# Kernel tuning notes

Hardware: AMD Instinct MI355X
Metric: run time of the kernel (lower is better)

Reference implementation:

```python
import jax, jax.numpy as jnp
import numpy as np

N = 50000   # nodes
E = 300000  # directed edges (~Delaunay mesh, degree 6)
H = 128     # hidden_size
TW = 5      # time_window
P = 3       # process_steps
NODE_IN = 9
EDGE_IN = 4
LN_EPS = 1e-5


def _ln(x, g, b):
    m = jnp.mean(x, axis=-1, keepdims=True)
    v = jnp.var(x, axis=-1, keepdims=True)
    return (x - m) * jax.lax.rsqrt(v + LN_EPS) * g + b


def _mlp_ln(x, w1, b1, w2, b2, g, bb):
    # Linear -> ReLU -> Linear -> LayerNorm (matches MLP(..., layer_norm=True))
    h = jax.nn.relu(x @ w1 + b1)
    return _ln(h @ w2 + b2, g, bb)


def setup_inputs() -> dict:
    key = jax.random.key(0)
    ks = iter(jax.random.split(key, 64))
    def nrm(shape):
        return jax.random.normal(next(ks), shape, jnp.float32)
    def lin(fi, fo, stack=None):
        sh = (fi, fo) if stack is None else (stack, fi, fo)
        return nrm(sh) / np.sqrt(fi)
    inp = {}
    inp["temperature"] = nrm((N,))
    inp["temperature_prev"] = nrm((N,))
    inp["heat_source"] = nrm((N,))
    inp["heat_source_prev"] = nrm((N,))
    inp["heat_source_next"] = nrm((N, TW))
    inp["mesh_pos"] = jax.random.uniform(next(ks), (N, 2), jnp.float32)
    inp["edge_index"] = jax.random.randint(next(ks), (2, E), 0, N, jnp.int32)
    # Normalizer params (running mean/std)
    inp["node_norm_mean"] = jnp.zeros((NODE_IN,), jnp.float32)
    inp["node_norm_std"] = jnp.ones((NODE_IN,), jnp.float32)
    inp["edge_norm_mean"] = jnp.zeros((EDGE_IN,), jnp.float32)
    inp["edge_norm_std"] = jnp.ones((EDGE_IN,), jnp.float32)
    # node encoder
    inp["ne_w1"] = lin(NODE_IN, H); inp["ne_b1"] = jnp.zeros((H,), jnp.float32)
    inp["ne_w2"] = lin(H, H);       inp["ne_b2"] = jnp.zeros((H,), jnp.float32)
    inp["ne_g"] = jnp.ones((H,), jnp.float32); inp["ne_be"] = jnp.zeros((H,), jnp.float32)
    # edge encoder
    inp["ee_w1"] = lin(EDGE_IN, H); inp["ee_b1"] = jnp.zeros((H,), jnp.float32)
    inp["ee_w2"] = lin(H, H);       inp["ee_b2"] = jnp.zeros((H,), jnp.float32)
    inp["ee_g"] = jnp.ones((H,), jnp.float32); inp["ee_be"] = jnp.zeros((H,), jnp.float32)
    # processors (stacked over P steps): edge_mlp in=3H, node_mlp in=2H
    inp["pe_w1"] = lin(3 * H, H, P); inp["pe_b1"] = jnp.zeros((P, H), jnp.float32)
    inp["pe_w2"] = lin(H, H, P);     inp["pe_b2"] = jnp.zeros((P, H), jnp.float32)
    inp["pe_g"] = jnp.ones((P, H), jnp.float32); inp["pe_be"] = jnp.zeros((P, H), jnp.float32)
    inp["pn_w1"] = lin(2 * H, H, P); inp["pn_b1"] = jnp.zeros((P, H), jnp.float32)
    inp["pn_w2"] = lin(H, H, P);     inp["pn_b2"] = jnp.zeros((P, H), jnp.float32)
    inp["pn_g"] = jnp.ones((P, H), jnp.float32); inp["pn_be"] = jnp.zeros((P, H), jnp.float32)
    # decoder (Conv1d kernel_size=1 == per-node Linear), Swish in between
    inp["dec_w1"] = lin(H, H // 2); inp["dec_b1"] = jnp.zeros((H // 2,), jnp.float32)
    inp["dec_w2"] = lin(H // 2, TW); inp["dec_b2"] = jnp.zeros((TW,), jnp.float32)
    return inp


def reference(temperature, temperature_prev, heat_source, heat_source_prev,
              heat_source_next, mesh_pos, edge_index,
              node_norm_mean, node_norm_std, edge_norm_mean, edge_norm_std,
              ne_w1, ne_b1, ne_w2, ne_b2, ne_g, ne_be,
              ee_w1, ee_b1, ee_w2, ee_b2, ee_g, ee_be,
              pe_w1, pe_b1, pe_w2, pe_b2, pe_g, pe_be,
              pn_w1, pn_b1, pn_w2, pn_b2, pn_g, pn_be,
              dec_w1, dec_b1, dec_w2, dec_b2):
    u = temperature
    # node features: [u, u_dot, q, q_dot, q_next]  -> [N, 9]
    x = jnp.concatenate([
        u[:, None], (u - temperature_prev)[:, None],
        heat_source[:, None], (heat_source - heat_source_prev)[:, None],
        heat_source_next], axis=-1)
    s, r = edge_index[0], edge_index[1]  # senders (source j), receivers (target i)
    rel = mesh_pos[s] - mesh_pos[r]                       # [E, 2]
    dist = jnp.linalg.norm(rel, axis=-1, keepdims=True)   # [E, 1]
    relt = (u[s] - u[r])[:, None]                         # [E, 1]
    e = jnp.concatenate([rel, dist, relt], axis=-1)       # [E, 4]

    xh = _mlp_ln((x - node_norm_mean) / node_norm_std, ne_w1, ne_b1, ne_w2, ne_b2, ne_g, ne_be)
    eh = _mlp_ln((e - edge_norm_mean) / edge_norm_std, ee_w1, ee_b1, ee_w2, ee_b2, ee_g, ee_be)

    n_nodes = xh.shape[0]
    for i in range(P):
        xs, xr = xh[s], xh[r]  # x_j = x[source], x_i = x[target]
        # message: edge_mlp(cat[x_i, x_j, e]) then scatter-add at target index
        msg = _mlp_ln(jnp.concatenate([xr, xs, eh], axis=-1),
                      pe_w1[i], pe_b1[i], pe_w2[i], pe_b2[i], pe_g[i], pe_be[i])
        aggr = jax.ops.segment_sum(msg, r, num_segments=n_nodes)
        # node update + residual
        new_x = _mlp_ln(jnp.concatenate([aggr, xh], axis=-1),
                        pn_w1[i], pn_b1[i], pn_w2[i], pn_b2[i], pn_g[i], pn_be[i]) + xh
        # edge update (note row/col ordering differs from message) + residual
        new_e = _mlp_ln(jnp.concatenate([xs, xr, eh], axis=-1),
                        pe_w1[i], pe_b1[i], pe_w2[i], pe_b2[i], pe_g[i], pe_be[i]) + eh
        xh, eh = new_x, new_e

    # decoder: 1x1 convs == per-node linears, Swish(beta=1) activation
    h = xh @ dec_w1 + dec_b1
    h = h * jax.nn.sigmoid(h)
    delta = (h @ dec_w2 + dec_b2).reshape(-1, TW)
    dt = jnp.arange(1, TW + 1, dtype=delta.dtype)
    return dt[None, :] * delta
```

## Files before the change

kernel.cpp:

```cpp
#include <hip/hip_runtime.h>
#include <stdint.h>

typedef unsigned short u16;
typedef __attribute__((ext_vector_type(8))) short bf16x8_t;
typedef __attribute__((ext_vector_type(4))) float f32x4_t;

__device__ __forceinline__ float bl(u16 x) {
  union { unsigned u; float f; } c; c.u = ((unsigned)x) << 16; return c.f;
}
__device__ __forceinline__ u16 fb(float x) {
  union { float f; unsigned u; } c; c.f = x;
  unsigned r = c.u + 0x7fffu + ((c.u >> 16) & 1u);
  return (u16)(r >> 16);
}

__global__ void sentinel_kernel(float* out, int n) {
  int i = blockIdx.x * 256 + threadIdx.x;
  if (i < n) out[i] = 12345.f;
}

struct TSeg { const float* src; u16* dst; };
struct TArgs { TSeg s[23]; };
__global__ void transpose_w(TArgs a) {
  const float* src = a.s[blockIdx.x].src;
  u16* dst = a.s[blockIdx.x].dst;
  for (int e = threadIdx.x; e < 16384; e += 256) {
    int n = e >> 7, k = e & 127;
    dst[e] = fb(src[k * 128 + n]);
  }
}

__global__ void zero_i32(int* p, int n) {
  int i = blockIdx.x * 256 + threadIdx.x;
  if (i < n) p[i] = 0;
}
__global__ void deg_count(const int* __restrict__ ei, int* __restrict__ cnt, int E) {
  int e = blockIdx.x * 256 + threadIdx.x;
  if (e < E) atomicAdd(&cnt[ei[E + e]], 1);
}
__global__ void scan1(const int* __restrict__ cnt, int* __restrict__ part,
                      int* __restrict__ bsum, int N) {
  __shared__ int s[256];
  int i = blockIdx.x * 256 + threadIdx.x;
  s[threadIdx.x] = (i < N) ? cnt[i] : 0;
  __syncthreads();
#pragma unroll
  for (int o = 1; o < 256; o <<= 1) {
    int t = (threadIdx.x >= o) ? s[threadIdx.x - o] : 0;
    __syncthreads();
    s[threadIdx.x] += t;
    __syncthreads();
  }
  if (i < N) part[i] = s[threadIdx.x];
  if (threadIdx.x == 255) bsum[blockIdx.x] = s[255];
}
__global__ void scan2(int* bsum, int nb) {
  if (threadIdx.x == 0 && blockIdx.x == 0) {
    int acc = 0;
    for (int i = 0; i < nb; ++i) { int t = bsum[i]; bsum[i] = acc; acc += t; }
  }
}
__global__ void scan3(const int* __restrict__ part, const int* __restrict__ bsum,
                      int* __restrict__ start, int N) {
  int i = blockIdx.x * 256 + threadIdx.x;
  if (i < N) start[i + 1] = part[i] + bsum[i >> 8];
  if (i == 0) start[0] = 0;
}
__global__ void fill_slot(const int* __restrict__ ei, int* __restrict__ cnt2,
                          const int* __restrict__ start, int* __restrict__ sortedS,
                          int* __restrict__ sortedR, int E) {
  int e = blockIdx.x * 256 + threadIdx.x;
  if (e >= E) return;
  int s = ei[e], r = ei[E + e];
  int p = atomicAdd(&cnt2[r], 1);
  int slot = start[r] + p;
  sortedS[slot] = s;
  sortedR[slot] = r;
}

__global__ void node_feat_kernel(const float* __restrict__ t, const float* __restrict__ tp,
                                 const float* __restrict__ q, const float* __restrict__ qp,
                                 const float* __restrict__ qn, const float* __restrict__ nm,
                                 const float* __restrict__ ns, float* __restrict__ nfeat,
                                 int n_nodes) {
  int n = blockIdx.x * 256 + threadIdx.x;
  if (n >= n_nodes) return;
  float u = t[n];
  float x[9];
  x[0] = u; x[1] = u - tp[n];
  float hq = q[n];
  x[2] = hq; x[3] = hq - qp[n];
#pragma unroll
  for (int j = 0; j < 5; ++j) x[4 + j] = qn[n * 5 + j];
#pragma unroll
  for (int k = 0; k < 9; ++k) nfeat[n * 9 + k] = (x[k] - nm[k]) / ns[k];
}

__global__ void edge_feat_kernel(const int* __restrict__ sArr, const int* __restrict__ rArr,
                                 const float* __restrict__ mp, const float* __restrict__ u,
                                 const float* __restrict__ em, const float* __restrict__ es,
                                 float* __restrict__ efeat, int n_edges) {
  int e = blockIdx.x * 256 + threadIdx.x;
  if (e >= n_edges) return;
  int s = sArr[e], r = rArr[e];
  float rx = mp[s * 2] - mp[r * 2];
  float ry = mp[s * 2 + 1] - mp[r * 2 + 1];
  float d = sqrtf(rx * rx + ry * ry);
  float rt = u[s] - u[r];
  float x[4] = {rx, ry, d, rt};
#pragma unroll
  for (int k = 0; k < 4; ++k) efeat[e * 4 + k] = (x[k] - em[k]) / es[k];
}

template <int K>
__global__ __launch_bounds__(256, 2) void encode_fused(
    const float* __restrict__ feat, const float* __restrict__ w1f, const float* __restrict__ b1f,
    const u16* __restrict__ wt2, const float* __restrict__ b2, const float* __restrict__ gg,
    const float* __restrict__ bb, u16* __restrict__ out, int M) {
  __shared__ float sW1[K * 128];
  __shared__ float sB1[128];
  __shared__ u16 sH[64][136];
  const int tid = threadIdx.x;
  const int wave = tid >> 6, lane = tid & 63;
  const int q = lane >> 4, l16 = lane & 15;
  const int m0 = blockIdx.x * 64;
  const int rowb = wave * 16 + q * 4;
  const int arow = m0 + wave * 16 + l16;
  const int arc = arow < M ? arow : M - 1;

  for (int i = tid; i < K * 128; i += 256) sW1[i] = w1f[i];
  if (tid < 128) sB1[tid] = b1f[tid];
  __syncthreads();

  float fr[K];
#pragma unroll
  for (int k = 0; k < K; ++k) fr[k] = feat[(size_t)arc * K + k];

  f32x4_t acc[8];
#pragma unroll
  for (int b = 0; b < 8; ++b) acc[b] = (f32x4_t){0.f, 0.f, 0.f, 0.f};
#pragma unroll
  for (int kk = 0; kk < 4; ++kk) {
    union { u16 u[8]; bf16x8_t v; } cv;
#pragma unroll
    for (int j = 0; j < 8; ++j) {
      int col = kk * 32 + q * 8 + j;
      float h = sB1[col];
#pragma unroll
      for (int k = 0; k < K; ++k) h += fr[k] * sW1[k * 128 + col];
      cv.u[j] = fb(h > 0.f ? h : 0.f);
    }
#pragma unroll
    for (int nt = 0; nt < 8; ++nt) {
      bf16x8_t bfv = *(const bf16x8_t*)(wt2 + (size_t)(nt * 16 + l16) * 128 + kk * 32 + q * 8);
      acc[nt] = __builtin_amdgcn_mfma_f32_16x16x32_bf16(cv.v, bfv, acc[nt], 0, 0, 0);
    }
  }

  float bcol[8], gcol[8], becol[8];
#pragma unroll
  for (int nt = 0; nt < 8; ++nt) {
    bcol[nt] = b2[nt * 16 + l16];
    gcol[nt] = gg[nt * 16 + l16];
    becol[nt] = bb[nt * 16 + l16];
  }
  float s[4] = {0, 0, 0, 0}, ss[4] = {0, 0, 0, 0};
#pragma unroll
  for (int r = 0; r < 4; ++r)
#pragma unroll
    for (int nt = 0; nt < 8; ++nt) {
      float v = acc[nt][r] + bcol[nt];
      s[r] += v;
      ss[r] += v * v;
    }
#pragma unroll
  for (int r = 0; r < 4; ++r) {
#pragma unroll
    for (int m = 1; m <= 8; m <<= 1) {
      s[r] += __shfl_xor(s[r], m, 64);
      ss[r] += __shfl_xor(ss[r], m, 64);
    }
  }
#pragma unroll
  for (int r = 0; r < 4; ++r) {
    float mean = s[r] * (1.f / 128.f);
    float var = fmaxf(ss[r] * (1.f / 128.f) - mean * mean, 0.f);
    float rstd = rsqrtf(var + 1e-5f);
#pragma unroll
    for (int nt = 0; nt < 8; ++nt) {
      float v = (acc[nt][r] + bcol[nt] - mean) * rstd * gcol[nt] + becol[nt];
      sH[rowb + r][nt * 16 + l16] = fb(v);
    }
  }
  __syncthreads();
#pragma unroll
  for (int it = 0; it < 4; ++it) {
    int lin = it * 256 + tid;
    int row = lin >> 4, ch = (lin & 15) * 8;
    int grow = m0 + row;
    if (grow >= M) continue;
    *(uint4*)(out + (size_t)grow * 128 + ch) = *(uint4*)(&sH[row][ch]);
  }
}

__global__ __launch_bounds__(256, 2) void gemm64_2w(
    const u16* __restrict__ A, const u16* __restrict__ WT0, const u16* __restrict__ WT1,
    u16* __restrict__ out0, u16* __restrict__ out1, float* __restrict__ aggr, int M) {
  __shared__ u16 sO0[64][136];
  __shared__ u16 sO1[64][136];
  const int tid = threadIdx.x;
  const int wave = tid >> 6, lane = tid & 63;
  const int q = lane >> 4, l16 = lane & 15;
  const int m0 = blockIdx.x * 64;
  int arow = m0 + wave * 16 + l16;
  if (arow >= M) arow = M - 1;

  {
    float4 z = make_float4(0.f, 0.f, 0.f, 0.f);
#pragma unroll
    for (int it = 0; it < 8; ++it) {
      int lin = it * 256 + tid;
      int row = lin >> 5, c4 = (lin & 31) * 4;
      int grow = m0 + row;
      if (grow < M) *(float4*)(aggr + (size_t)grow * 128 + c4) = z;
    }
  }

  f32x4_t a0[8], a1[8];
#pragma unroll
  for (int b = 0; b < 8; ++b) {
    a0[b] = (f32x4_t){0.f, 0.f, 0.f, 0.f};
    a1[b] = (f32x4_t){0.f, 0.f, 0.f, 0.f};
  }
#pragma unroll 2
  for (int kk = 0; kk < 4; ++kk) {
    bf16x8_t af = *(const bf16x8_t*)(A + (size_t)arow * 128 + kk * 32 + q * 8);
#pragma unroll
    for (int nt = 0; nt < 8; ++nt) {
      bf16x8_t b0 = *(const bf16x8_t*)(WT0 + (size_t)(nt * 16 + l16) * 128 + kk * 32 + q * 8);
      bf16x8_t b1v = *(const bf16x8_t*)(WT1 + (size_t)(nt * 16 + l16) * 128 + kk * 32 + q * 8);
      a0[nt] = __builtin_amdgcn_mfma_f32_16x16x32_bf16(af, b0, a0[nt], 0, 0, 0);
      a1[nt] = __builtin_amdgcn_mfma_f32_16x16x32_bf16(af, b1v, a1[nt], 0, 0, 0);
    }
  }
  const int rowb = wave * 16 + q * 4;
#pragma unroll
  for (int r = 0; r < 4; ++r)
#pragma unroll
    for (int nt = 0; nt < 8; ++nt) {
      sO0[rowb + r][nt * 16 + l16] = fb(a0[nt][r]);
      sO1[rowb + r][nt * 16 + l16] = fb(a1[nt][r]);
    }
  __syncthreads();
#pragma unroll
  for (int it = 0; it < 4; ++it) {
    int lin = it * 256 + tid;
    int row = lin >> 4, ch = (lin & 15) * 8;
    int grow = m0 + row;
    if (grow >= M) continue;
    *(uint4*)(out0 + (size_t)grow * 128 + ch) = *(uint4*)(&sO0[row][ch]);
    *(uint4*)(out1 + (size_t)grow * 128 + ch) = *(uint4*)(&sO1[row][ch]);
  }
}

__global__ __launch_bounds__(256, 2) void node_fused_2w(
    u16* __restrict__ xh, float* __restrict__ aggr, const u16* __restrict__ wtA,
    const u16* __restrict__ wtB, const float* __restrict__ b1, const u16* __restrict__ wt2,
    const float* __restrict__ b2, const float* __restrict__ gg, const float* __restrict__ bb,
    const u16* __restrict__ wtA2, const u16* __restrict__ wtB2, u16* __restrict__ xhA,
    u16* __restrict__ xhB, int M) {
  __shared__ u16 sH[64][136];
  __shared__ u16 sO1[64][136];
  const int tid = threadIdx.x;
  const int wave = tid >> 6, lane = tid & 63;
  const int q = lane >> 4, l16 = lane & 15;
  const int m0 = blockIdx.x * 64;
  const int rowb = wave * 16 + q * 4;
  const int arow = m0 + wave * 16 + l16;
  const int arc = arow < M ? arow : M - 1;

  bf16x8_t xf[4], af_[4];
#pragma unroll
  for (int kk = 0; kk < 4; ++kk) {
    xf[kk] = *(const bf16x8_t*)(xh + (size_t)arc * 128 + kk * 32 + q * 8);
    const float* ap = aggr + (size_t)arc * 128 + kk * 32 + q * 8;
    union { u16 u[8]; bf16x8_t v; } cv;
#pragma unroll
    for (int j = 0; j < 8; ++j) cv.u[j] = fb(ap[j]);
    af_[kk] = cv.v;
  }

  f32x4_t acc[8];
#pragma unroll
  for (int b = 0; b < 8; ++b) acc[b] = (f32x4_t){0.f, 0.f, 0.f, 0.f};
#pragma unroll
  for (int kk = 0; kk < 4; ++kk) {
#pragma unroll
    for (int nt = 0; nt < 8; ++nt) {
      bf16x8_t bA = *(const bf16x8_t*)(wtA + (size_t)(nt * 16 + l16) * 128 + kk * 32 + q * 8);
      bf16x8_t bB = *(const bf16x8_t*)(wtB + (size_t)(nt * 16 + l16) * 128 + kk * 32 + q * 8);
      acc[nt] = __builtin_amdgcn_mfma_f32_16x16x32_bf16(af_[kk], bA, acc[nt], 0, 0, 0);
      acc[nt] = __builtin_amdgcn_mfma_f32_16x16x32_bf16(xf[kk], bB, acc[nt], 0, 0, 0);
    }
  }
  float bcol1[8];
#pragma unroll
  for (int nt = 0; nt < 8; ++nt) bcol1[nt] = b1[nt * 16 + l16];
#pragma unroll
  for (int r = 0; r < 4; ++r)
#pragma unroll
    for (int nt = 0; nt < 8; ++nt) {
      float v = acc[nt][r] + bcol1[nt];
      sH[rowb + r][nt * 16 + l16] = fb(v > 0.f ? v : 0.f);
    }
  __syncthreads();

  f32x4_t acc2[8];
#pragma unroll
  for (int b = 0; b < 8; ++b) acc2[b] = (f32x4_t){0.f, 0.f, 0.f, 0.f};
#pragma unroll
  for (int kk = 0; kk < 4; ++kk) {
    bf16x8_t afm = *(const bf16x8_t*)(&sH[wave * 16 + l16][kk * 32 + q * 8]);
#pragma unroll
    for (int nt = 0; nt < 8; ++nt) {
      bf16x8_t bfv = *(const bf16x8_t*)(wt2 + (size_t)(nt * 16 + l16) * 128 + kk * 32 + q * 8);
      acc2[nt] = __builtin_amdgcn_mfma_f32_16x16x32_bf16(afm, bfv, acc2[nt], 0, 0, 0);
    }
  }
  float bcol[8], gcol[8], becol[8];
#pragma unroll
  for (int nt = 0; nt < 8; ++nt) {
    bcol[nt] = b2[nt * 16 + l16];
    gcol[nt] = gg[nt * 16 + l16];
    becol[nt] = bb[nt * 16 + l16];
  }
  float s[4] = {0, 0, 0, 0}, ss[4] = {0, 0, 0, 0};
#pragma unroll
  for (int r = 0; r < 4; ++r)
#pragma unroll
    for (int nt = 0; nt < 8; ++nt) {
      float v = acc2[nt][r] + bcol[nt];
      s[r] += v;
      ss[r] += v * v;
    }
#pragma unroll
  for (int r = 0; r < 4; ++r) {
#pragma unroll
    for (int m = 1; m <= 8; m <<= 1) {
      s[r] += __shfl_xor(s[r], m, 64);
      ss[r] += __shfl_xor(ss[r], m, 64);
    }
  }
  __syncthreads();
#pragma unroll
  for (int r = 0; r < 4; ++r) {
    float mean = s[r] * (1.f / 128.f);
    float var = fmaxf(ss[r] * (1.f / 128.f) - mean * mean, 0.f);
    float rstd = rsqrtf(var + 1e-5f);
#pragma unroll
    for (int nt = 0; nt < 8; ++nt) {
      float v = (acc2[nt][r] + bcol[nt] - mean) * rstd * gcol[nt] + becol[nt];
      sH[rowb + r][nt * 16 + l16] = fb(v);
    }
  }
  __syncthreads();

  bf16x8_t nf[4];
#pragma unroll
  for (int kk = 0; kk < 4; ++kk) {
    u16 y8[8];
    *(uint4*)y8 = *(uint4*)(&sH[wave * 16 + l16][kk * 32 + q * 8]);
#pragma unroll
    for (int j = 0; j < 8; ++j) y8[j] = fb(bl(y8[j]) + bl((u16)xf[kk][j]));
    nf[kk] = *(bf16x8_t*)y8;
    if (arow < M)
      *(uint4*)(xh + (size_t)arow * 128 + kk * 32 + q * 8) = *(uint4*)y8;
  }

  if (wtA2 == nullptr) return;

  if (arow < M) {
    float4 z = make_float4(0.f, 0.f, 0.f, 0.f);
#pragma unroll
    for (int kk = 0; kk < 4; ++kk) {
      *(float4*)(aggr + (size_t)arow * 128 + kk * 32 + q * 8) = z;
      *(float4*)(aggr + (size_t)arow * 128 + kk * 32 + q * 8 + 4) = z;
    }
  }

  f32x4_t a0[8], a1[8];
#pragma unroll
  for (int b = 0; b < 8; ++b) {
    a0[b] = (f32x4_t){0.f, 0.f, 0.f, 0.f};
    a1[b] = (f32x4_t){0.f, 0.f, 0.f, 0.f};
  }
#pragma unroll
  for (int kk = 0; kk < 4; ++kk) {
#pragma unroll
    for (int nt = 0; nt < 8; ++nt) {
      bf16x8_t b0 = *(const bf16x8_t*)(wtA2 + (size_t)(nt * 16 + l16) * 128 + kk * 32 + q * 8);
      bf16x8_t b1v = *(const bf16x8_t*)(wtB2 + (size_t)(nt * 16 + l16) * 128 + kk * 32 + q * 8);
      a0[nt] = __builtin_amdgcn_mfma_f32_16x16x32_bf16(nf[kk], b0, a0[nt], 0, 0, 0);
      a1[nt] = __builtin_amdgcn_mfma_f32_16x16x32_bf16(nf[kk], b1v, a1[nt], 0, 0, 0);
    }
  }
  __syncthreads();
#pragma unroll
  for (int r = 0; r < 4; ++r)
#pragma unroll
    for (int nt = 0; nt < 8; ++nt) {
      sH[rowb + r][nt * 16 + l16] = fb(a0[nt][r]);
      sO1[rowb + r][nt * 16 + l16] = fb(a1[nt][r]);
    }
  __syncthreads();
#pragma unroll
  for (int it = 0; it < 4; ++it) {
    int lin = it * 256 + tid;
    int row = lin >> 4, ch = (lin & 15) * 8;
    int grow = m0 + row;
    if (grow >= M) continue;
    *(uint4*)(xhA + (size_t)grow * 128 + ch) = *(uint4*)(&sH[row][ch]);
    *(uint4*)(xhB + (size_t)grow * 128 + ch) = *(uint4*)(&sO1[row][ch]);
  }
}

template <bool CSR>
__global__ __launch_bounds__(256, 2) void edge_fused(
    u16* __restrict__ eh, const u16* __restrict__ xhA, const u16* __restrict__ xhB,
    const u16* __restrict__ wtC, const float* __restrict__ b1, const u16* __restrict__ wt2,
    const float* __restrict__ b2, const float* __restrict__ gg, const float* __restrict__ bb,
    const int* __restrict__ sArr, const int* __restrict__ rArr,
    const int* __restrict__ startp, float* __restrict__ aggr, int E) {
  __shared__ u16 sHm[64][136];
  __shared__ u16 sHe[64][136];
  __shared__ int sR[64];
  const int tid = threadIdx.x;
  const int wave = tid >> 6, lane = tid & 63;
  const int q = lane >> 4, l16 = lane & 15;
  const int m0 = blockIdx.x * 64;
  const int rowb = wave * 16 + q * 4;
  int arow = m0 + wave * 16 + l16;
  int arc = arow < E ? arow : E - 1;

  if (tid < 64) {
    int e = m0 + tid;
    sR[tid] = (e < E) ? rArr[e] : -1;
  }

  int prow[4], pch[4], pr_[4];
  uint4 pAs[4], pBs[4];
#pragma unroll
  for (int it = 0; it < 4; ++it) {
    int lin = it * 256 + tid;
    prow[it] = lin >> 4;
    pch[it] = (lin & 15) * 8;
    int ge = m0 + prow[it];
    int gc = ge < E ? ge : E - 1;
    int ps = sArr[gc];
    pr_[it] = rArr[gc];
    pAs[it] = *(const uint4*)(xhA + (size_t)ps * 128 + pch[it]);
    pBs[it] = *(const uint4*)(xhB + (size_t)ps * 128 + pch[it]);
  }
  bf16x8_t ehf[4];
#pragma unroll
  for (int kk = 0; kk < 4; ++kk)
    ehf[kk] = *(const bf16x8_t*)(eh + (size_t)arc * 128 + kk * 32 + q * 8);

  f32x4_t accC[8];
#pragma unroll
  for (int b = 0; b < 8; ++b) accC[b] = (f32x4_t){0.f, 0.f, 0.f, 0.f};
#pragma unroll
  for (int kk = 0; kk < 4; ++kk) {
#pragma unroll
    for (int nt = 0; nt < 8; ++nt) {
      bf16x8_t bfv = *(const bf16x8_t*)(wtC + (size_t)(nt * 16 + l16) * 128 + kk * 32 + q * 8);
      accC[nt] = __builtin_amdgcn_mfma_f32_16x16x32_bf16(ehf[kk], bfv, accC[nt], 0, 0, 0);
    }
  }
#pragma unroll
  for (int r = 0; r < 4; ++r)
#pragma unroll
    for (int nt = 0; nt < 8; ++nt) sHm[rowb + r][nt * 16 + l16] = fb(accC[nt][r]);
  __syncthreads();

#pragma unroll
  for (int it = 0; it < 4; ++it) {
    int row = prow[it], ch = pch[it];
    bool ok = (m0 + row) < E;
    int r_ = pr_[it] >= 0 ? pr_[it] : 0;
    u16 t8[8], ar[8], as_[8], br[8], bs[8], hm[8], he[8];
    *(uint4*)t8 = *(uint4*)(&sHm[row][ch]);
    *(uint4*)ar = *(const uint4*)(xhA + (size_t)r_ * 128 + ch);
    *(uint4*)br = *(const uint4*)(xhB + (size_t)r_ * 128 + ch);
    *(uint4*)as_ = pAs[it];
    *(uint4*)bs = pBs[it];
#pragma unroll
    for (int j = 0; j < 8; ++j) {
      float t = bl(t8[j]) + b1[ch + j];
      float vm = t + bl(ar[j]) + bl(bs[j]);
      float ve = t + bl(as_[j]) + bl(br[j]);
      hm[j] = (ok && vm > 0.f) ? fb(vm) : 0;
      he[j] = (ok && ve > 0.f) ? fb(ve) : 0;
    }
    *(uint4*)(&sHm[row][ch]) = *(uint4*)hm;
    *(uint4*)(&sHe[row][ch]) = *(uint4*)he;
  }
  __syncthreads();

  float bcol[8], gcol[8], becol[8];
#pragma unroll
  for (int nt = 0; nt < 8; ++nt) {
    bcol[nt] = b2[nt * 16 + l16];
    gcol[nt] = gg[nt * 16 + l16];
    becol[nt] = bb[nt * 16 + l16];
  }

  f32x4_t accM[8], accE[8];
#pragma unroll
  for (int b = 0; b < 8; ++b) {
    accM[b] = (f32x4_t){0.f, 0.f, 0.f, 0.f};
    accE[b] = (f32x4_t){0.f, 0.f, 0.f, 0.f};
  }
#pragma unroll
  for (int kk = 0; kk < 4; ++kk) {
    bf16x8_t afm = *(const bf16x8_t*)(&sHm[wave * 16 + l16][kk * 32 + q * 8]);
    bf16x8_t afe = *(const bf16x8_t*)(&sHe[wave * 16 + l16][kk * 32 + q * 8]);
#pragma unroll
    for (int nt = 0; nt < 8; ++nt) {
      bf16x8_t bfv = *(const bf16x8_t*)(wt2 + (size_t)(nt * 16 + l16) * 128 + kk * 32 + q * 8);
      accM[nt] = __builtin_amdgcn_mfma_f32_16x16x32_bf16(afm, bfv, accM[nt], 0, 0, 0);
      accE[nt] = __builtin_amdgcn_mfma_f32_16x16x32_bf16(afe, bfv, accE[nt], 0, 0, 0);
    }
  }
  float sm[4] = {0, 0, 0, 0}, ssm[4] = {0, 0, 0, 0};
  float se[4] = {0, 0, 0, 0}, sse[4] = {0, 0, 0, 0};
#pragma unroll
  for (int r = 0; r < 4; ++r)
#pragma unroll
    for (int nt = 0; nt < 8; ++nt) {
      float vm = accM[nt][r] + bcol[nt];
      float ve = accE[nt][r] + bcol[nt];
      sm[r] += vm; ssm[r] += vm * vm;
      se[r] += ve; sse[r] += ve * ve;
    }
#pragma unroll
  for (int r = 0; r < 4; ++r) {
#pragma unroll
    for (int m = 1; m <= 8; m <<= 1) {
      sm[r] += __shfl_xor(sm[r], m, 64);
      ssm[r] += __shfl_xor(ssm[r], m, 64);
      se[r] += __shfl_xor(se[r], m, 64);
      sse[r] += __shfl_xor(sse[r], m, 64);
    }
  }

  if (!CSR) {
#pragma unroll
    for (int r = 0; r < 4; ++r) {
      int row = m0 + rowb + r;
      if (row >= E) continue;
      int rr = sR[rowb + r];
      float mean = sm[r] * (1.f / 128.f);
      float var = fmaxf(ssm[r] * (1.f / 128.f) - mean * mean, 0.f);
      float rstd = rsqrtf(var + 1e-5f);
#pragma unroll
      for (int nt = 0; nt < 8; ++nt) {
        float v = (accM[nt][r] + bcol[nt] - mean) * rstd * gcol[nt] + becol[nt];
        atomicAdd(&aggr[(size_t)rr * 128 + nt * 16 + l16], v);
      }
    }
  }

  __syncthreads();
#pragma unroll
  for (int r = 0; r < 4; ++r) {
    float meanE = se[r] * (1.f / 128.f);
    float varE = fmaxf(sse[r] * (1.f / 128.f) - meanE * meanE, 0.f);
    float rstdE = rsqrtf(varE + 1e-5f);
    float meanM = sm[r] * (1.f / 128.f);
    float varM = fmaxf(ssm[r] * (1.f / 128.f) - meanM * meanM, 0.f);
    float rstdM = rsqrtf(varM + 1e-5f);
#pragma unroll
    for (int nt = 0; nt < 8; ++nt) {
      float ve = (accE[nt][r] + bcol[nt] - meanE) * rstdE * gcol[nt] + becol[nt];
      sHe[rowb + r][nt * 16 + l16] = fb(ve);
      if (CSR) {
        float vm = (accM[nt][r] + bcol[nt] - meanM) * rstdM * gcol[nt] + becol[nt];
        sHm[rowb + r][nt * 16 + l16] = fb(vm);
      }
    }
  }
  __syncthreads();

#pragma unroll
  for (int it = 0; it < 4; ++it) {
    int row = prow[it], ch = pch[it];
    int grow = m0 + row;
    if (grow >= E) continue;
    u16 y8[8], e8[8];
    *(uint4*)y8 = *(uint4*)(&sHe[row][ch]);
    *(uint4*)e8 = *(const uint4*)(eh + (size_t)grow * 128 + ch);
#pragma unroll
    for (int j = 0; j < 8; ++j) y8[j] = fb(bl(y8[j]) + bl(e8[j]));
    *(uint4*)(eh + (size_t)grow * 128 + ch) = *(uint4*)y8;

    if (CSR) {
      int rr = sR[row];
      bool first = (row == 0) || (sR[row - 1] != rr);
      if (!first) continue;
      int gs = startp[rr], ge2 = startp[rr + 1];
      int le = ge2 - m0;
      if (le > 64) le = 64;
      float acc[8] = {0, 0, 0, 0, 0, 0, 0, 0};
      for (int i = row; i < le; ++i) {
        u16 m8[8];
        *(uint4*)m8 = *(uint4*)(&sHm[i][ch]);
#pragma unroll
        for (int j = 0; j < 8; ++j) acc[j] += bl(m8[j]);
      }
      if (gs >= m0 && ge2 <= m0 + 64) {
        *(float4*)(aggr + (size_t)rr * 128 + ch) = make_float4(acc[0], acc[1], acc[2], acc[3]);
        *(float4*)(aggr + (size_t)rr * 128 + ch + 4) =
            make_float4(acc[4], acc[5], acc[6], acc[7]);
      } else {
#pragma unroll
        for (int j = 0; j < 8; ++j) atomicAdd(&aggr[(size_t)rr * 128 + ch + j], acc[j]);
      }
    }
  }
}

__global__ void decoder_kernel(const u16* __restrict__ xh, const float* __restrict__ w1,
                               const float* __restrict__ b1, const float* __restrict__ w2,
                               const float* __restrict__ b2, float* __restrict__ out,
                               int n_nodes) {
  __shared__ float sx[4][128];
  int tid = threadIdx.x;
  int lw = tid >> 6, lane = tid & 63;
  int n0 = blockIdx.x * 4;
  for (int i = tid; i < 512; i += 256) {
    int nn = i >> 7, c = i & 127;
    int n = n0 + nn;
    sx[nn][c] = (n < n_nodes) ? bl(xh[(size_t)n * 128 + c]) : 0.f;
  }
  __syncthreads();
  int n = n0 + lw;
  float h = b1[lane];
#pragma unroll 16
  for (int k = 0; k < 128; ++k) h += sx[lw][k] * w1[k * 64 + lane];
  float hs = h * (1.f / (1.f + __expf(-h)));
  float d[5];
#pragma unroll
  for (int t = 0; t < 5; ++t) {
    float p = hs * w2[lane * 5 + t];
#pragma unroll
    for (int m = 1; m <= 32; m <<= 1) p += __shfl_xor(p, m, 64);
    d[t] = p;
  }
  if (lane == 0 && n < n_nodes) {
#pragma unroll
    for (int t = 0; t < 5; ++t)
      out[(size_t)n * 5 + t] = (float)(t + 1) * (d[t] + b2[t]);
  }
}

extern "C" void kernel_launch(void* const* d_in, const int* in_sizes, int n_in, void* d_out,
                              int out_size, void* d_ws, size_t ws_size, hipStream_t stream) {
  auto F = [&](int i) { return (const float*)d_in[i]; };
  const int* edge_index = (const int*)d_in[6];
  const int N_ = in_sizes[0];
  const int E_ = in_sizes[6] / 2;

  char* wsb = (char*)d_ws;
  size_t off = 0;
  auto alloc = [&](size_t bytes) -> char* {
    char* p = wsb + off;
    off += (bytes + 255) & ~(size_t)255;
    return p;
  };
  u16* xh = (u16*)alloc((size_t)N_ * 128 * 2);
  u16* xhA = (u16*)alloc((size_t)N_ * 128 * 2);
  u16* xhB = (u16*)alloc((size_t)N_ * 128 * 2);
  u16* ehP = (u16*)alloc((size_t)E_ * 128 * 2);
  float* aggr = (float*)alloc((size_t)N_ * 128 * 4);
  float* nfeat = (float*)xhA;
  float* efeat = (float*)xhB;
  u16* wne2T = (u16*)alloc(16384 * 2);
  u16* wee2T = (u16*)alloc(16384 * 2);
  u16* wpe1T = (u16*)alloc((size_t)9 * 16384 * 2);
  u16* wpe2T = (u16*)alloc((size_t)3 * 16384 * 2);
  u16* wpn1T = (u16*)alloc((size_t)6 * 16384 * 2);
  u16* wpn2T = (u16*)alloc((size_t)3 * 16384 * 2);

  const size_t base_off = off;
  int* startp = (int*)alloc((size_t)(N_ + 1) * 4);
  int* cntp = (int*)alloc((size_t)N_ * 4);
  int* partp = (int*)alloc((size_t)N_ * 4);
  int* bsump = (int*)alloc(((size_t)(N_ + 255) / 256) * 4 + 256);
  int* sortedS = (int*)alloc((size_t)E_ * 4);
  int* sortedR = (int*)alloc((size_t)E_ * 4);
  bool useCSR = (off <= ws_size);
  if (!useCSR) {
    off = base_off;
    if (off > ws_size) {
      sentinel_kernel<<<(out_size + 255) / 256, 256, 0, stream>>>((float*)d_out, out_size);
      return;
    }
  }

  TArgs ta;
  int ts = 0;
  ta.s[ts++] = {F(13), wne2T};
  ta.s[ts++] = {F(19), wee2T};
  for (int i = 0; i < 3; ++i)
    for (int b = 0; b < 3; ++b)
      ta.s[ts++] = {F(23) + (size_t)(i * 3 + b) * 16384, wpe1T + (size_t)(i * 3 + b) * 16384};
  for (int i = 0; i < 3; ++i) ta.s[ts++] = {F(25) + (size_t)i * 16384, wpe2T + (size_t)i * 16384};
  for (int i = 0; i < 3; ++i)
    for (int b = 0; b < 2; ++b)
      ta.s[ts++] = {F(29) + (size_t)(i * 2 + b) * 16384, wpn1T + (size_t)(i * 2 + b) * 16384};
  for (int i = 0; i < 3; ++i) ta.s[ts++] = {F(31) + (size_t)i * 16384, wpn2T + (size_t)i * 16384};

  const int tilesN = (N_ + 63) / 64;
  const int tilesE = (E_ + 63) / 64;
  const int nb = (N_ + 255) / 256;
  dim3 blk(256);

  transpose_w<<<23, blk, 0, stream>>>(ta);

  const int* sArr = edge_index;
  const int* rArr = edge_index + E_;
  if (useCSR) {
    zero_i32<<<(N_ + 255) / 256, blk, 0, stream>>>(cntp, N_);
    deg_count<<<(E_ + 255) / 256, blk, 0, stream>>>(edge_index, cntp, E_);
    scan1<<<nb, blk, 0, stream>>>(cntp, partp, bsump, N_);
    scan2<<<1, blk, 0, stream>>>(bsump, nb);
    scan3<<<nb, blk, 0, stream>>>(partp, bsump, startp, N_);
    zero_i32<<<(N_ + 255) / 256, blk, 0, stream>>>(cntp, N_);
    fill_slot<<<(E_ + 255) / 256, blk, 0, stream>>>(edge_index, cntp, startp, sortedS, sortedR,
                                                    E_);
    sArr = sortedS;
    rArr = sortedR;
  }

  node_feat_kernel<<<(N_ + 255) / 256, blk, 0, stream>>>(F(0), F(1), F(2), F(3), F(4), F(7),
                                                         F(8), nfeat, N_);
  encode_fused<9><<<tilesN, blk, 0, stream>>>(nfeat, F(11), F(12), wne2T, F(14), F(15), F(16),
                                              xh, N_);
  edge_feat_kernel<<<(E_ + 255) / 256, blk, 0, stream>>>(sArr, rArr, F(5), F(0), F(9), F(10),
                                                         efeat, E_);
  encode_fused<4><<<tilesE, blk, 0, stream>>>(efeat, F(17), F(18), wee2T, F(20), F(21), F(22),
                                              ehP, E_);

  for (int i = 0; i < 3; ++i) {
    const u16* wtA = wpe1T + (size_t)(i * 3 + 0) * 16384;
    const u16* wtB = wpe1T + (size_t)(i * 3 + 1) * 16384;
    const u16* wtC = wpe1T + (size_t)(i * 3 + 2) * 16384;
    const float* pb1 = F(24) + i * 128;
    const u16* wt2 = wpe2T + (size_t)i * 16384;
    const float* pb2 = F(26) + i * 128;
    const float* pg = F(27) + i * 128;
    const float* pbe = F(28) + i * 128;
    const u16* wtnA = wpn1T + (size_t)(i * 2 + 0) * 16384;
    const u16* wtnB = wpn1T + (size_t)(i * 2 + 1) * 16384;
    const float* nb1 = F(30) + i * 128;
    const u16* wtn2 = wpn2T + (size_t)i * 16384;
    const float* nb2 = F(32) + i * 128;
    const float* ng = F(33) + i * 128;
    const float* nbe = F(34) + i * 128;

    if (i == 0)
      gemm64_2w<<<tilesN, blk, 0, stream>>>(xh, wtA, wtB, xhA, xhB, aggr, N_);
    if (useCSR) {
      edge_fused<true><<<tilesE, blk, 0, stream>>>(ehP, xhA, xhB, wtC, pb1, wt2, pb2, pg, pbe,
                                                   sArr, rArr, startp, aggr, E_);
    } else {
      edge_fused<false><<<tilesE, blk, 0, stream>>>(ehP, xhA, xhB, wtC, pb1, wt2, pb2, pg, pbe,
                                                    sArr, rArr, nullptr, aggr, E_);
    }
    const u16* wtA2 = (i < 2) ? wpe1T + (size_t)((i + 1) * 3 + 0) * 16384 : nullptr;
    const u16* wtB2 = (i < 2) ? wpe1T + (size_t)((i + 1) * 3 + 1) * 16384 : nullptr;
    node_fused_2w<<<tilesN, blk, 0, stream>>>(xh, aggr, wtnA, wtnB, nb1, wtn2, nb2, ng, nbe,
                                              wtA2, wtB2, xhA, xhB, N_);
  }

  decoder_kernel<<<(N_ + 3) / 4, blk, 0, stream>>>(xh, F(35), F(36), F(37), F(38),
                                                   (float*)d_out, N_);
}
```

Baseline: 1.212 ms.

## Skip dead edge-update work in final step, parallelize scan and weight transpose

Adds a LAST template flag to the fused edge kernel so the final processor step skips the edge-update branch. Its output is never consumed, so the extra gathers, the second GEMM, the LayerNorm and the eh write-back are dropped. The edge residual write-back now reuses the eh fragments already held in registers instead of re-reading eh from global memory. Separately, the single-thread block-sum scan becomes a block-parallel scan, and the weight transpose goes through shared memory for coalesced reads. These setup-kernel changes add some synchronization and code complexity.

Result: no change. 1.218 ms (+0.5%).

```diff
diff --git a/kernel.cpp b/kernel.cpp
--- a/kernel.cpp
+++ b/kernel.cpp
@@ -22,11 +22,17 @@
 struct TSeg { const float* src; u16* dst; };
 struct TArgs { TSeg s[23]; };
 __global__ void transpose_w(TArgs a) {
+  __shared__ u16 sT[128][132];
   const float* src = a.s[blockIdx.x].src;
   u16* dst = a.s[blockIdx.x].dst;
   for (int e = threadIdx.x; e < 16384; e += 256) {
+    int k = e >> 7, n = e & 127;
+    sT[n][k] = fb(src[e]);
+  }
+  __syncthreads();
+  for (int e = threadIdx.x; e < 16384; e += 256) {
     int n = e >> 7, k = e & 127;
-    dst[e] = fb(src[k * 128 + n]);
+    dst[e] = sT[n][k];
   }
 }
 
@@ -55,9 +61,27 @@
   if (threadIdx.x == 255) bsum[blockIdx.x] = s[255];
 }
 __global__ void scan2(int* bsum, int nb) {
-  if (threadIdx.x == 0 && blockIdx.x == 0) {
-    int acc = 0;
-    for (int i = 0; i < nb; ++i) { int t = bsum[i]; bsum[i] = acc; acc += t; }
+  __shared__ int s[256];
+  __shared__ int carry;
+  if (threadIdx.x == 0) carry = 0;
+  __syncthreads();
+  for (int base = 0; base < nb; base += 256) {
+    int i = base + threadIdx.x;
+    int v = (i < nb) ? bsum[i] : 0;
+    s[threadIdx.x] = v;
+    __syncthreads();
+#pragma unroll
+    for (int o = 1; o < 256; o <<= 1) {
+      int t = (threadIdx.x >= o) ? s[threadIdx.x - o] : 0;
+      __syncthreads();
+      s[threadIdx.x] += t;
+      __syncthreads();
+    }
+    int exc = s[threadIdx.x] - v + carry;
+    if (i < nb) bsum[i] = exc;
+    __syncthreads();
+    if (threadIdx.x == 255) carry += s[255];
+    __syncthreads();
   }
 }
 __global__ void scan3(const int* __restrict__ part, const int* __restrict__ bsum,
@@ -424,7 +448,7 @@
   }
 }
 
-template <bool CSR>
+template <bool CSR, bool LAST>
 __global__ __launch_bounds__(256, 2) void edge_fused(
     u16* __restrict__ eh, const u16* __restrict__ xhA, const u16* __restrict__ xhB,
     const u16* __restrict__ wtC, const float* __restrict__ b1, const u16* __restrict__ wt2,
@@ -432,7 +456,7 @@
     const int* __restrict__ sArr, const int* __restrict__ rArr,
     const int* __restrict__ startp, float* __restrict__ aggr, int E) {
   __shared__ u16 sHm[64][136];
-  __shared__ u16 sHe[64][136];
+  __shared__ u16 sHe[LAST ? 1 : 64][136];
   __shared__ int sR[64];
   const int tid = threadIdx.x;
   const int wave = tid >> 6, lane = tid & 63;
@@ -458,7 +482,7 @@
     int gc = ge < E ? ge : E - 1;
     int ps = sArr[gc];
     pr_[it] = rArr[gc];
-    pAs[it] = *(const uint4*)(xhA + (size_t)ps * 128 + pch[it]);
+    if constexpr (!LAST) pAs[it] = *(const uint4*)(xhA + (size_t)ps * 128 + pch[it]);
     pBs[it] = *(const uint4*)(xhB + (size_t)ps * 128 + pch[it]);
   }
   bf16x8_t ehf[4];
@@ -491,19 +515,23 @@
     u16 t8[8], ar[8], as_[8], br[8], bs[8], hm[8], he[8];
     *(uint4*)t8 = *(uint4*)(&sHm[row][ch]);
     *(uint4*)ar = *(const uint4*)(xhA + (size_t)r_ * 128 + ch);
-    *(uint4*)br = *(const uint4*)(xhB + (size_t)r_ * 128 + ch);
-    *(uint4*)as_ = pAs[it];
+    if constexpr (!LAST) {
+      *(uint4*)br = *(const uint4*)(xhB + (size_t)r_ * 128 + ch);
+      *(uint4*)as_ = pAs[it];
+    }
     *(uint4*)bs = pBs[it];
 #pragma unroll
     for (int j = 0; j < 8; ++j) {
       float t = bl(t8[j]) + b1[ch + j];
       float vm = t + bl(ar[j]) + bl(bs[j]);
-      float ve = t + bl(as_[j]) + bl(br[j]);
       hm[j] = (ok && vm > 0.f) ? fb(vm) : 0;
-      he[j] = (ok && ve > 0.f) ? fb(ve) : 0;
+      if constexpr (!LAST) {
+        float ve = t + bl(as_[j]) + bl(br[j]);
+        he[j] = (ok && ve > 0.f) ? fb(ve) : 0;
+      }
     }
     *(uint4*)(&sHm[row][ch]) = *(uint4*)hm;
-    *(uint4*)(&sHe[row][ch]) = *(uint4*)he;
+    if constexpr (!LAST) *(uint4*)(&sHe[row][ch]) = *(uint4*)he;
   }
   __syncthreads();
 
@@ -524,12 +552,14 @@
 #pragma unroll
   for (int kk = 0; kk < 4; ++kk) {
     bf16x8_t afm = *(const bf16x8_t*)(&sHm[wave * 16 + l16][kk * 32 + q * 8]);
-    bf16x8_t afe = *(const bf16x8_t*)(&sHe[wave * 16 + l16][kk * 32 + q * 8]);
+    bf16x8_t afe;
+    if constexpr (!LAST) afe = *(const bf16x8_t*)(&sHe[wave * 16 + l16][kk * 32 + q * 8]);
 #pragma unroll
     for (int nt = 0; nt < 8; ++nt) {
       bf16x8_t bfv = *(const bf16x8_t*)(wt2 + (size_t)(nt * 16 + l16) * 128 + kk * 32 + q * 8);
       accM[nt] = __builtin_amdgcn_mfma_f32_16x16x32_bf16(afm, bfv, accM[nt], 0, 0, 0);
-      accE[nt] = __builtin_amdgcn_mfma_f32_16x16x32_bf16(afe, bfv, accE[nt], 0, 0, 0);
+      if constexpr (!LAST)
+        accE[nt] = __builtin_amdgcn_mfma_f32_16x16x32_bf16(afe, bfv, accE[nt], 0, 0, 0);
     }
   }
   float sm[4] = {0, 0, 0, 0}, ssm[4] = {0, 0, 0, 0};
@@ -539,9 +569,11 @@
 #pragma unroll
     for (int nt = 0; nt < 8; ++nt) {
       float vm = accM[nt][r] + bcol[nt];
-      float ve = accE[nt][r] + bcol[nt];
       sm[r] += vm; ssm[r] += vm * vm;
-      se[r] += ve; sse[r] += ve * ve;
+      if constexpr (!LAST) {
+        float ve = accE[nt][r] + bcol[nt];
+        se[r] += ve; sse[r] += ve * ve;
+      }
     }
 #pragma unroll
   for (int r = 0; r < 4; ++r) {
@@ -549,8 +581,10 @@
     for (int m = 1; m <= 8; m <<= 1) {
       sm[r] += __shfl_xor(sm[r], m, 64);
       ssm[r] += __shfl_xor(ssm[r], m, 64);
-      se[r] += __shfl_xor(se[r], m, 64);
-      sse[r] += __shfl_xor(sse[r], m, 64);
+      if constexpr (!LAST) {
+        se[r] += __shfl_xor(se[r], m, 64);
+        sse[r] += __shfl_xor(sse[r], m, 64);
+      }
     }
   }
 
@@ -574,17 +608,22 @@
   __syncthreads();
 #pragma unroll
   for (int r = 0; r < 4; ++r) {
-    float meanE = se[r] * (1.f / 128.f);
-    float varE = fmaxf(sse[r] * (1.f / 128.f) - meanE * meanE, 0.f);
-    float rstdE = rsqrtf(varE + 1e-5f);
     float meanM = sm[r] * (1.f / 128.f);
     float varM = fmaxf(ssm[r] * (1.f / 128.f) - meanM * meanM, 0.f);
     float rstdM = rsqrtf(varM + 1e-5f);
-#pragma unroll
-    for (int nt = 0; nt < 8; ++nt) {
-      float ve = (accE[nt][r] + bcol[nt] - meanE) * rstdE * gcol[nt] + becol[nt];
-      sHe[rowb + r][nt * 16 + l16] = fb(ve);
-      if (CSR) {
+    if constexpr (!LAST) {
+      float meanE = se[r] * (1.f / 128.f);
+      float varE = fmaxf(sse[r] * (1.f / 128.f) - meanE * meanE, 0.f);
+      float rstdE = rsqrtf(varE + 1e-5f);
+#pragma unroll
+      for (int nt = 0; nt < 8; ++nt) {
+        float ve = (accE[nt][r] + bcol[nt] - meanE) * rstdE * gcol[nt] + becol[nt];
+        sHe[rowb + r][nt * 16 + l16] = fb(ve);
+      }
+    }
+    if (CSR) {
+#pragma unroll
+      for (int nt = 0; nt < 8; ++nt) {
         float vm = (accM[nt][r] + bcol[nt] - meanM) * rstdM * gcol[nt] + becol[nt];
         sHm[rowb + r][nt * 16 + l16] = fb(vm);
       }
@@ -592,20 +631,26 @@
   }
   __syncthreads();
 
-#pragma unroll
-  for (int it = 0; it < 4; ++it) {
-    int row = prow[it], ch = pch[it];
-    int grow = m0 + row;
-    if (grow >= E) continue;
-    u16 y8[8], e8[8];
-    *(uint4*)y8 = *(uint4*)(&sHe[row][ch]);
-    *(uint4*)e8 = *(const uint4*)(eh + (size_t)grow * 128 + ch);
-#pragma unroll
-    for (int j = 0; j < 8; ++j) y8[j] = fb(bl(y8[j]) + bl(e8[j]));
-    *(uint4*)(eh + (size_t)grow * 128 + ch) = *(uint4*)y8;
-
-    if (CSR) {
+  if constexpr (!LAST) {
+#pragma unroll
+    for (int kk = 0; kk < 4; ++kk) {
+      u16 y8[8];
+      *(uint4*)y8 = *(uint4*)(&sHe[wave * 16 + l16][kk * 32 + q * 8]);
+#pragma unroll
+      for (int j = 0; j < 8; ++j) y8[j] = fb(bl(y8[j]) + bl((u16)ehf[kk][j]));
+      if (arow < E)
+        *(uint4*)(eh + (size_t)arow * 128 + kk * 32 + q * 8) = *(uint4*)y8;
+    }
+  }
+
+  if (CSR) {
+#pragma unroll
+    for (int it = 0; it < 4; ++it) {
+      int row = prow[it], ch = pch[it];
+      int grow = m0 + row;
+      if (grow >= E) continue;
       int rr = sR[row];
+      if (rr < 0) continue;
       bool first = (row == 0) || (sR[row - 1] != rr);
       if (!first) continue;
       int gs = startp[rr], ge2 = startp[rr + 1];
@@ -771,12 +816,21 @@
 
     if (i == 0)
       gemm64_2w<<<tilesN, blk, 0, stream>>>(xh, wtA, wtB, xhA, xhB, aggr, N_);
+    const bool last = (i == 2);
     if (useCSR) {
-      edge_fused<true><<<tilesE, blk, 0, stream>>>(ehP, xhA, xhB, wtC, pb1, wt2, pb2, pg, pbe,
-                                                   sArr, rArr, startp, aggr, E_);
+      if (last)
+        edge_fused<true, true><<<tilesE, blk, 0, stream>>>(ehP, xhA, xhB, wtC, pb1, wt2, pb2,
+                                                           pg, pbe, sArr, rArr, startp, aggr, E_);
+      else
+        edge_fused<true, false><<<tilesE, blk, 0, stream>>>(ehP, xhA, xhB, wtC, pb1, wt2, pb2,
+                                                            pg, pbe, sArr, rArr, startp, aggr, E_);
     } else {
-      edge_fused<false><<<tilesE, blk, 0, stream>>>(ehP, xhA, xhB, wtC, pb1, wt2, pb2, pg, pbe,
-                                                    sArr, rArr, nullptr, aggr, E_);
+      if (last)
+        edge_fused<false, true><<<tilesE, blk, 0, stream>>>(ehP, xhA, xhB, wtC, pb1, wt2, pb2,
+                                                            pg, pbe, sArr, rArr, nullptr, aggr, E_);
+      else
+        edge_fused<false, false><<<tilesE, blk, 0, stream>>>(ehP, xhA, xhB, wtC, pb1, wt2, pb2,
+                                                             pg, pbe, sArr, rArr, nullptr, aggr, E_);
     }
     const u16* wtA2 = (i < 2) ? wpe1T + (size_t)((i + 1) * 3 + 0) * 16384 : nullptr;
     const u16* wtB2 = (i < 2) ? wpe1T + (size_t)((i + 1) * 3 + 1) * 16384 : nullptr;
```
